# Kernel tuning notes

Hardware: AMD Instinct MI355X
Metric: run time of the kernel (lower is better)

The kernel has to match this reference:

```python
import jax, jax.numpy as jnp
import numpy as np

B, S, D, H = 2, 2048, 1024, 16
HD = D // H  # head_dim = 64


def setup_inputs() -> dict:
    key = jax.random.key(0)
    ks = jax.random.split(key, 6)
    std = 0.02
    return {
        "x": jax.random.normal(ks[0], (B, S, D), dtype=jnp.float32),
        "gamma": jnp.ones((D,), jnp.float32),
        "beta": jnp.zeros((D,), jnp.float32),
        "w_qkv": jax.random.normal(ks[1], (D, 3 * D), jnp.float32) * std,
        "b_qkv": jnp.zeros((3 * D,), jnp.float32),
        "w_out": jax.random.normal(ks[2], (D, D), jnp.float32) * std,
        "b_out": jnp.zeros((D,), jnp.float32),
        "w_gate": jax.random.normal(ks[3], (D, D), jnp.float32) * std,
        "b_gate": jnp.zeros((D,), jnp.float32),
    }


def reference(x, gamma, beta, w_qkv, b_qkv, w_out, b_out, w_gate, b_gate):
    residual = x
    # Pre-norm (LayerNorm over last dim, eps matches torch default 1e-5)
    mu = jnp.mean(x, axis=-1, keepdims=True)
    var = jnp.mean(jnp.square(x - mu), axis=-1, keepdims=True)
    xn = (x - mu) * jax.lax.rsqrt(var + 1e-5) * gamma + beta

    # Fused QKV projection: [B,S,3D] -> [B,S,3,H,HD]
    qkv = (xn @ w_qkv + b_qkv).reshape(B, S, 3, H, HD)
    q = qkv[:, :, 0].transpose(0, 2, 1, 3)  # [B,H,S,HD]
    k = qkv[:, :, 1].transpose(0, 2, 1, 3)
    v = qkv[:, :, 2].transpose(0, 2, 1, 3)

    scale = 1.0 / jnp.sqrt(jnp.float32(HD))
    scores = jnp.einsum("bhqd,bhkd->bhqk", q, k) * scale  # [B,H,S,S]
    attn = jax.nn.softmax(scores, axis=-1)  # dropout is identity in eval
    ctx = jnp.einsum("bhqk,bhkd->bhqd", attn, v)  # [B,H,S,HD]
    ctx = ctx.transpose(0, 2, 1, 3).reshape(B, S, D)

    out = ctx @ w_out + b_out
    gate = jax.nn.sigmoid(xn @ w_gate + b_gate)
    return out * gate + residual
```

## Files before the change

kernel.cpp:

```cpp
#include <hip/hip_runtime.h>

using u16 = unsigned short;
typedef __attribute__((ext_vector_type(8))) short bf16x8;
typedef __attribute__((ext_vector_type(4))) float f32x4;

constexpr int Bc = 2, Sc = 2048, Dc = 1024, Hc = 16;
constexpr int Mc = Bc * Sc;
constexpr int N3 = 3 * Dc;

__device__ __forceinline__ u16 f2bf(float f) {
  unsigned u = __float_as_uint(f);
  u += 0x7fffu + ((u >> 16) & 1u);
  return (u16)(u >> 16);
}

__device__ __forceinline__ void gload16(const void* g, void* l) {
  __builtin_amdgcn_global_load_lds(
      (const __attribute__((address_space(1))) void*)g,
      (__attribute__((address_space(3))) void*)l, 16, 0, 0);
}

__device__ __forceinline__ int swz(int row, int slot) {
  return row * 64 + ((slot ^ (row & 7)) << 3);
}

__global__ __launch_bounds__(256) void ln_kernel(
    const float* __restrict__ x, const float* __restrict__ gamma,
    const float* __restrict__ beta, u16* __restrict__ xn) {
  __shared__ float sred[8];
  const int row = blockIdx.x, tid = threadIdx.x;
  const float4 a = ((const float4*)(x + (size_t)row * Dc))[tid];
  float s = a.x + a.y + a.z + a.w;
  float ss = a.x * a.x + a.y * a.y + a.z * a.z + a.w * a.w;
#pragma unroll
  for (int off = 32; off; off >>= 1) {
    s += __shfl_xor(s, off, 64);
    ss += __shfl_xor(ss, off, 64);
  }
  const int wid = tid >> 6, lane = tid & 63;
  if (lane == 0) { sred[wid] = s; sred[4 + wid] = ss; }
  __syncthreads();
  s = sred[0] + sred[1] + sred[2] + sred[3];
  ss = sred[4] + sred[5] + sred[6] + sred[7];
  const float mean = s * (1.0f / Dc);
  const float rstd = rsqrtf(ss * (1.0f / Dc) - mean * mean + 1e-5f);
  const float4 g = ((const float4*)gamma)[tid];
  const float4 b = ((const float4*)beta)[tid];
  ushort4 o;
  o.x = f2bf((a.x - mean) * rstd * g.x + b.x);
  o.y = f2bf((a.y - mean) * rstd * g.y + b.y);
  o.z = f2bf((a.z - mean) * rstd * g.z + b.z);
  o.w = f2bf((a.w - mean) * rstd * g.w + b.w);
  *(ushort4*)(xn + (size_t)row * Dc + tid * 4) = o;
}

__global__ __launch_bounds__(256) void convertT(
    const float* __restrict__ W, u16* __restrict__ WT, int K, int N) {
  __shared__ float t[32][33];
  const int k0 = blockIdx.y * 32, n0 = blockIdx.x * 32;
  const int tid = threadIdx.x;
  const int r = tid >> 3, c4 = (tid & 7) << 2;
  const float4 v = *(const float4*)(W + (size_t)(k0 + r) * N + n0 + c4);
  t[r][c4 + 0] = v.x; t[r][c4 + 1] = v.y; t[r][c4 + 2] = v.z; t[r][c4 + 3] = v.w;
  __syncthreads();
  ushort4 o;
  o.x = f2bf(t[c4 + 0][r]); o.y = f2bf(t[c4 + 1][r]);
  o.z = f2bf(t[c4 + 2][r]); o.w = f2bf(t[c4 + 3][r]);
  *(ushort4*)(WT + (size_t)(n0 + r) * K + k0 + c4) = o;
}

__global__ __launch_bounds__(256) void gemm_qkv_kernel(
    const u16* __restrict__ A, const u16* __restrict__ BT,
    const float* __restrict__ bias, u16* __restrict__ Qb,
    u16* __restrict__ Kb, u16* __restrict__ VbT) {
  __shared__ __align__(16) u16 Al[128 * 64];
  __shared__ __align__(16) u16 Bl[128 * 64];
  const int tid = threadIdx.x, wv = tid >> 6, ln = tid & 63;
  const int bm = blockIdx.y * 128, bn = blockIdx.x * 128;
  const int wr = (wv >> 1) * 64, wc = (wv & 1) * 64;

  f32x4 acc[4][4];
#pragma unroll
  for (int i = 0; i < 4; i++)
#pragma unroll
    for (int j = 0; j < 4; j++) acc[i][j] = f32x4{0.f, 0.f, 0.f, 0.f};

  for (int k0 = 0; k0 < Dc; k0 += 64) {
    __syncthreads();
#pragma unroll
    for (int c = 0; c < 4; c++) {
      const int ci = wv + c * 4;
      const int i = ci * 64 + ln;
      const int row = i >> 3, slot = i & 7;
      const size_t go = (size_t)row * Dc + k0 + ((slot ^ (row & 7)) << 3);
      gload16(A + (size_t)bm * Dc + go, &Al[ci * 512]);
      gload16(BT + (size_t)bn * Dc + go, &Bl[ci * 512]);
    }
    __syncthreads();
#pragma unroll
    for (int ks = 0; ks < 2; ks++) {
      bf16x8 af[4], bfr[4];
#pragma unroll
      for (int m = 0; m < 4; m++)
        af[m] = *(const bf16x8*)&Al[swz(wr + m * 16 + (ln & 15), ks * 4 + (ln >> 4))];
#pragma unroll
      for (int n = 0; n < 4; n++)
        bfr[n] = *(const bf16x8*)&Bl[swz(wc + n * 16 + (ln & 15), ks * 4 + (ln >> 4))];
#pragma unroll
      for (int m = 0; m < 4; m++)
#pragma unroll
        for (int n = 0; n < 4; n++)
          acc[m][n] = __builtin_amdgcn_mfma_f32_16x16x32_bf16(af[m], bfr[n], acc[m][n], 0, 0, 0);
    }
  }

  const int fq = ln >> 4, fr = ln & 15;
#pragma unroll
  for (int mi = 0; mi < 4; mi++) {
    const int row = bm + wr + mi * 16 + fq * 4;
    const int b = row >> 11, sl = row & 2047;
#pragma unroll
    for (int ni = 0; ni < 4; ni++) {
      const int col = bn + wc + ni * 16 + fr;
      const int which = col >> 10, h = (col >> 6) & 15, hd = col & 63;
      const int bh = b * Hc + h;
      const float bs = bias[col];
      if (which == 0) {
#pragma unroll
        for (int r = 0; r < 4; r++)
          Qb[((size_t)bh * Sc + sl + r) * 64 + hd] = f2bf((acc[mi][ni][r] + bs) * 0.125f);
      } else if (which == 1) {
#pragma unroll
        for (int r = 0; r < 4; r++)
          Kb[((size_t)bh * Sc + sl + r) * 64 + hd] = f2bf(acc[mi][ni][r] + bs);
      } else {
        ushort4 st;
        st.x = f2bf(acc[mi][ni][0] + bs); st.y = f2bf(acc[mi][ni][1] + bs);
        st.z = f2bf(acc[mi][ni][2] + bs); st.w = f2bf(acc[mi][ni][3] + bs);
        *(ushort4*)&VbT[((size_t)bh * 64 + hd) * Sc + sl] = st;
      }
    }
  }
}

__global__ __launch_bounds__(256) void attn_kernel(
    const u16* __restrict__ Qb, const u16* __restrict__ Kb,
    const u16* __restrict__ VbT, u16* __restrict__ ctx) {
  __shared__ __align__(16) u16 Ks[64 * 64];
  __shared__ __align__(16) u16 Vs[64 * 64];
  __shared__ __align__(16) u16 Pl[4][16 * 64];
  const int tid = threadIdx.x, wv = tid >> 6, ln = tid & 63;
  const int qt = blockIdx.x, bh = blockIdx.y;
  const int b = bh >> 4, h = bh & 15;
  const int q0 = qt * 64 + wv * 16;

  bf16x8 qf[2];
  {
    const u16* Qrow = Qb + ((size_t)bh * Sc + q0 + (ln & 15)) * 64;
    qf[0] = *(const bf16x8*)(Qrow + ((ln >> 4) << 3));
    qf[1] = *(const bf16x8*)(Qrow + 32 + ((ln >> 4) << 3));
  }

  f32x4 O[4];
  float m_[4], l_[4];
#pragma unroll
  for (int f = 0; f < 4; f++) O[f] = f32x4{0.f, 0.f, 0.f, 0.f};
#pragma unroll
  for (int r = 0; r < 4; r++) { m_[r] = -1e30f; l_[r] = 0.f; }

  const u16* Kbase = Kb + (size_t)bh * Sc * 64;
  const u16* Vbase = VbT + (size_t)bh * 64 * Sc;
  u16* Pw = &Pl[wv][0];

  for (int kt = 0; kt < Sc / 64; kt++) {
    __syncthreads();
#pragma unroll
    for (int c = 0; c < 2; c++) {
      const int ci = wv + c * 4;
      const int i = ci * 64 + ln;
      const int row = i >> 3, slot = i & 7;
      const int so = (slot ^ (row & 7)) << 3;
      gload16(Kbase + ((size_t)kt * 64 + row) * 64 + so, &Ks[ci * 512]);
      gload16(Vbase + (size_t)row * Sc + kt * 64 + so, &Vs[ci * 512]);
    }
    __syncthreads();

    f32x4 sf[4];
#pragma unroll
    for (int f = 0; f < 4; f++) {
      f32x4 s = f32x4{0.f, 0.f, 0.f, 0.f};
#pragma unroll
      for (int ks = 0; ks < 2; ks++) {
        bf16x8 kf = *(const bf16x8*)&Ks[swz(f * 16 + (ln & 15), ks * 4 + (ln >> 4))];
        s = __builtin_amdgcn_mfma_f32_16x16x32_bf16(qf[ks], kf, s, 0, 0, 0);
      }
      sf[f] = s;
    }

    float al[4];
#pragma unroll
    for (int r = 0; r < 4; r++) {
      float v = fmaxf(fmaxf(sf[0][r], sf[1][r]), fmaxf(sf[2][r], sf[3][r]));
#pragma unroll
      for (int o = 1; o < 16; o <<= 1) v = fmaxf(v, __shfl_xor(v, o, 16));
      const float mn = fmaxf(m_[r], v);
      al[r] = __expf(m_[r] - mn);
      m_[r] = mn;
    }
    float rs[4] = {0.f, 0.f, 0.f, 0.f};
#pragma unroll
    for (int f = 0; f < 4; f++)
#pragma unroll
      for (int r = 0; r < 4; r++) {
        const float p = __expf(sf[f][r] - m_[r]);
        sf[f][r] = p;
        rs[r] += p;
      }
#pragma unroll
    for (int r = 0; r < 4; r++) {
#pragma unroll
      for (int o = 1; o < 16; o <<= 1) rs[r] += __shfl_xor(rs[r], o, 16);
      l_[r] = l_[r] * al[r] + rs[r];
    }
#pragma unroll
    for (int f = 0; f < 4; f++)
#pragma unroll
      for (int r = 0; r < 4; r++) O[f][r] *= al[r];

#pragma unroll
    for (int f = 0; f < 4; f++)
#pragma unroll
      for (int r = 0; r < 4; r++) {
        const int row = (ln >> 4) * 4 + r, key = f * 16 + (ln & 15);
        Pw[row * 64 + (key ^ ((row & 7) << 3))] = f2bf(sf[f][r]);
      }
    asm volatile("s_waitcnt lgkmcnt(0)" ::: "memory");

#pragma unroll
    for (int f = 0; f < 4; f++)
#pragma unroll
      for (int ks = 0; ks < 2; ks++) {
        bf16x8 pa = *(const bf16x8*)&Pw[swz(ln & 15, ks * 4 + (ln >> 4))];
        bf16x8 vb = *(const bf16x8*)&Vs[swz(f * 16 + (ln & 15), ks * 4 + (ln >> 4))];
        O[f] = __builtin_amdgcn_mfma_f32_16x16x32_bf16(pa, vb, O[f], 0, 0, 0);
      }
  }

#pragma unroll
  for (int r = 0; r < 4; r++) l_[r] = 1.0f / l_[r];
#pragma unroll
  for (int f = 0; f < 4; f++)
#pragma unroll
    for (int r = 0; r < 4; r++) {
      const int row = q0 + (ln >> 4) * 4 + r;
      ctx[((size_t)b * Sc + row) * Dc + h * 64 + f * 16 + (ln & 15)] =
          f2bf(O[f][r] * l_[r]);
    }
}

__global__ __launch_bounds__(256) void final_kernel(
    const u16* __restrict__ ctx, const u16* __restrict__ xn,
    const u16* __restrict__ woutT, const u16* __restrict__ wgateT,
    const float* __restrict__ b_out, const float* __restrict__ b_gate,
    const float* __restrict__ x, float* __restrict__ out) {
  __shared__ __align__(16) u16 A1[64 * 64], A2[64 * 64], B1[64 * 64], B2[64 * 64];
  const int tid = threadIdx.x, wv = tid >> 6, ln = tid & 63;
  const int bm = blockIdx.y * 64, bn = blockIdx.x * 64;
  const int wr = (wv >> 1) * 32, wc = (wv & 1) * 32;

  f32x4 ac1[2][2], ac2[2][2];
#pragma unroll
  for (int i = 0; i < 2; i++)
#pragma unroll
    for (int j = 0; j < 2; j++) {
      ac1[i][j] = f32x4{0.f, 0.f, 0.f, 0.f};
      ac2[i][j] = f32x4{0.f, 0.f, 0.f, 0.f};
    }

  for (int k0 = 0; k0 < Dc; k0 += 64) {
    __syncthreads();
#pragma unroll
    for (int c = 0; c < 2; c++) {
      const int ci = wv + c * 4;
      const int i = ci * 64 + ln;
      const int row = i >> 3, slot = i & 7;
      const size_t go = (size_t)row * Dc + k0 + ((slot ^ (row & 7)) << 3);
      gload16(ctx + (size_t)bm * Dc + go, &A1[ci * 512]);
      gload16(xn + (size_t)bm * Dc + go, &A2[ci * 512]);
      gload16(woutT + (size_t)bn * Dc + go, &B1[ci * 512]);
      gload16(wgateT + (size_t)bn * Dc + go, &B2[ci * 512]);
    }
    __syncthreads();
#pragma unroll
    for (int ks = 0; ks < 2; ks++) {
      bf16x8 fa1[2], fa2[2], fb1[2], fb2[2];
#pragma unroll
      for (int m = 0; m < 2; m++) {
        const int off = swz(wr + m * 16 + (ln & 15), ks * 4 + (ln >> 4));
        fa1[m] = *(const bf16x8*)&A1[off];
        fa2[m] = *(const bf16x8*)&A2[off];
      }
#pragma unroll
      for (int n = 0; n < 2; n++) {
        const int off = swz(wc + n * 16 + (ln & 15), ks * 4 + (ln >> 4));
        fb1[n] = *(const bf16x8*)&B1[off];
        fb2[n] = *(const bf16x8*)&B2[off];
      }
#pragma unroll
      for (int m = 0; m < 2; m++)
#pragma unroll
        for (int n = 0; n < 2; n++) {
          ac1[m][n] = __builtin_amdgcn_mfma_f32_16x16x32_bf16(fa1[m], fb1[n], ac1[m][n], 0, 0, 0);
          ac2[m][n] = __builtin_amdgcn_mfma_f32_16x16x32_bf16(fa2[m], fb2[n], ac2[m][n], 0, 0, 0);
        }
    }
  }

  const int fq = ln >> 4, fr = ln & 15;
#pragma unroll
  for (int m = 0; m < 2; m++)
#pragma unroll
    for (int n = 0; n < 2; n++) {
      const int col = bn + wc + n * 16 + fr;
      const float bo = b_out[col], bg = b_gate[col];
#pragma unroll
      for (int r = 0; r < 4; r++) {
        const int row = bm + wr + m * 16 + fq * 4 + r;
        const float o = ac1[m][n][r] + bo;
        const float gv = ac2[m][n][r] + bg;
        const float sig = 1.0f / (1.0f + __expf(-gv));
        out[(size_t)row * Dc + col] = o * sig + x[(size_t)row * Dc + col];
      }
    }
}

extern "C" void kernel_launch(void* const* d_in, const int* in_sizes, int n_in,
                              void* d_out, int out_size, void* d_ws, size_t ws_size,
                              hipStream_t stream) {
  const float* x = (const float*)d_in[0];
  const float* gamma = (const float*)d_in[1];
  const float* beta = (const float*)d_in[2];
  const float* w_qkv = (const float*)d_in[3];
  const float* b_qkv = (const float*)d_in[4];
  const float* w_out = (const float*)d_in[5];
  const float* b_out = (const float*)d_in[6];
  const float* w_gate = (const float*)d_in[7];
  const float* b_gate = (const float*)d_in[8];
  float* out = (float*)d_out;

  u16* xn = (u16*)d_ws;
  u16* wqkvT = xn + (size_t)Mc * Dc;
  u16* woutT = wqkvT + (size_t)N3 * Dc;
  u16* wgateT = woutT + (size_t)Dc * Dc;
  u16* Qb = wgateT + (size_t)Dc * Dc;
  u16* Kb = Qb + (size_t)Bc * Hc * Sc * 64;
  u16* VbT = Kb + (size_t)Bc * Hc * Sc * 64;
  u16* ctxb = VbT + (size_t)Bc * Hc * Sc * 64;

  ln_kernel<<<Mc, 256, 0, stream>>>(x, gamma, beta, xn);
  convertT<<<dim3(N3 / 32, Dc / 32), 256, 0, stream>>>(w_qkv, wqkvT, Dc, N3);
  convertT<<<dim3(Dc / 32, Dc / 32), 256, 0, stream>>>(w_out, woutT, Dc, Dc);
  convertT<<<dim3(Dc / 32, Dc / 32), 256, 0, stream>>>(w_gate, wgateT, Dc, Dc);
  gemm_qkv_kernel<<<dim3(N3 / 128, Mc / 128), 256, 0, stream>>>(
      xn, wqkvT, b_qkv, Qb, Kb, VbT);
  attn_kernel<<<dim3(Sc / 64, Bc * Hc), 256, 0, stream>>>(Qb, Kb, VbT, ctxb);
  final_kernel<<<dim3(Dc / 64, Mc / 64), 256, 0, stream>>>(
      ctxb, xn, woutT, wgateT, b_out, b_gate, x, out);
}
```

Measured before the change: 287.5 us.

## Double-buffer attention K/V, lazy softmax rescale, XCD swizzle, larger final tiles

The attention kernel now runs 2 waves per block, each handling 32 query rows, and double-buffers K/V tiles in LDS so the next tile loads while the current one is computed. Softmax uses exp2 with log2e folded into the Q scale, and only rescales the running max when it grows past a threshold. Row sums are reduced once at the end instead of every tile. The QKV and final GEMMs remap blocks across XCDs, and the final GEMM uses 128-row tiles. This trades more registers and LDS per block, and fewer threads per block, for better overlap of loads and compute and less softmax work.

```diff
diff --git a/kernel.cpp b/kernel.cpp
--- a/kernel.cpp
+++ b/kernel.cpp
@@ -22,6 +22,14 @@
 
 __device__ __forceinline__ int swz(int row, int slot) {
   return row * 64 + ((slot ^ (row & 7)) << 3);
+}
+
+__device__ __forceinline__ void xcd_swizzle(int& bx, int& by) {
+  const int nwg = gridDim.x * gridDim.y;
+  const int bid = by * gridDim.x + bx;
+  const int s = (bid & 7) * (nwg >> 3) + (bid >> 3);
+  bx = s % gridDim.x;
+  by = s / gridDim.x;
 }
 
 __global__ __launch_bounds__(256) void ln_kernel(
@@ -76,7 +84,9 @@
   __shared__ __align__(16) u16 Al[128 * 64];
   __shared__ __align__(16) u16 Bl[128 * 64];
   const int tid = threadIdx.x, wv = tid >> 6, ln = tid & 63;
-  const int bm = blockIdx.y * 128, bn = blockIdx.x * 128;
+  int bxi = blockIdx.x, byi = blockIdx.y;
+  xcd_swizzle(bxi, byi);
+  const int bm = byi * 128, bn = bxi * 128;
   const int wr = (wv >> 1) * 64, wc = (wv & 1) * 64;
 
   f32x4 acc[4][4];
@@ -128,7 +138,8 @@
       if (which == 0) {
 #pragma unroll
         for (int r = 0; r < 4; r++)
-          Qb[((size_t)bh * Sc + sl + r) * 64 + hd] = f2bf((acc[mi][ni][r] + bs) * 0.125f);
+          Qb[((size_t)bh * Sc + sl + r) * 64 + hd] =
+              f2bf((acc[mi][ni][r] + bs) * 0.18033688011112042f);
       } else if (which == 1) {
 #pragma unroll
         for (int r = 0; r < 4; r++)
@@ -143,119 +154,165 @@
   }
 }
 
-__global__ __launch_bounds__(256) void attn_kernel(
+__global__ __launch_bounds__(128) void attn_kernel(
     const u16* __restrict__ Qb, const u16* __restrict__ Kb,
     const u16* __restrict__ VbT, u16* __restrict__ ctx) {
-  __shared__ __align__(16) u16 Ks[64 * 64];
-  __shared__ __align__(16) u16 Vs[64 * 64];
-  __shared__ __align__(16) u16 Pl[4][16 * 64];
+  __shared__ __align__(16) u16 Ks[2][64 * 64];
+  __shared__ __align__(16) u16 Vs[2][64 * 64];
+  __shared__ __align__(16) u16 Pl[2][32 * 64];
   const int tid = threadIdx.x, wv = tid >> 6, ln = tid & 63;
   const int qt = blockIdx.x, bh = blockIdx.y;
   const int b = bh >> 4, h = bh & 15;
-  const int q0 = qt * 64 + wv * 16;
-
-  bf16x8 qf[2];
-  {
-    const u16* Qrow = Qb + ((size_t)bh * Sc + q0 + (ln & 15)) * 64;
-    qf[0] = *(const bf16x8*)(Qrow + ((ln >> 4) << 3));
-    qf[1] = *(const bf16x8*)(Qrow + 32 + ((ln >> 4) << 3));
-  }
-
-  f32x4 O[4];
-  float m_[4], l_[4];
-#pragma unroll
-  for (int f = 0; f < 4; f++) O[f] = f32x4{0.f, 0.f, 0.f, 0.f};
-#pragma unroll
-  for (int r = 0; r < 4; r++) { m_[r] = -1e30f; l_[r] = 0.f; }
+  const int q0 = qt * 64 + wv * 32;
+  constexpr float THR = 11.5f;
+
+  bf16x8 qf[2][2];
+#pragma unroll
+  for (int a = 0; a < 2; a++)
+#pragma unroll
+    for (int ks = 0; ks < 2; ks++)
+      qf[a][ks] = *(const bf16x8*)(Qb + ((size_t)bh * Sc + q0 + a * 16 + (ln & 15)) * 64 +
+                                   (ks * 4 + (ln >> 4)) * 8);
+
+  f32x4 O[2][4];
+  float m_[2][4], l_[2][4];
+#pragma unroll
+  for (int a = 0; a < 2; a++)
+#pragma unroll
+    for (int f = 0; f < 4; f++) O[a][f] = f32x4{0.f, 0.f, 0.f, 0.f};
+#pragma unroll
+  for (int a = 0; a < 2; a++)
+#pragma unroll
+    for (int r = 0; r < 4; r++) { m_[a][r] = -1e30f; l_[a][r] = 0.f; }
 
   const u16* Kbase = Kb + (size_t)bh * Sc * 64;
   const u16* Vbase = VbT + (size_t)bh * 64 * Sc;
   u16* Pw = &Pl[wv][0];
 
+  int rk[4], rv[4];
+#pragma unroll
+  for (int c = 0; c < 4; c++) {
+    const int ci = wv * 4 + c;
+    const int i = ci * 64 + ln;
+    const int row = i >> 3, slot = i & 7;
+    const int so = (slot ^ (row & 7)) << 3;
+    rk[c] = row * 64 + so;
+    rv[c] = row * Sc + so;
+  }
+
+  auto stage = [&](int buf, int kt) {
+#pragma unroll
+    for (int c = 0; c < 4; c++) {
+      const int ci = wv * 4 + c;
+      gload16(Kbase + (size_t)kt * 4096 + rk[c], &Ks[buf][ci * 512]);
+      gload16(Vbase + (size_t)kt * 64 + rv[c], &Vs[buf][ci * 512]);
+    }
+  };
+
+  stage(0, 0);
+  asm volatile("s_waitcnt vmcnt(0)" ::: "memory");
+  __syncthreads();
+
   for (int kt = 0; kt < Sc / 64; kt++) {
+    const int cur = kt & 1;
+    if (kt + 1 < Sc / 64) stage(cur ^ 1, kt + 1);
+
+    f32x4 sf[2][4];
+#pragma unroll
+    for (int a = 0; a < 2; a++)
+#pragma unroll
+      for (int f = 0; f < 4; f++) sf[a][f] = f32x4{0.f, 0.f, 0.f, 0.f};
+    __builtin_amdgcn_s_setprio(1);
+#pragma unroll
+    for (int f = 0; f < 4; f++)
+#pragma unroll
+      for (int ks = 0; ks < 2; ks++) {
+        const bf16x8 kf = *(const bf16x8*)&Ks[cur][swz(f * 16 + (ln & 15), ks * 4 + (ln >> 4))];
+#pragma unroll
+        for (int a = 0; a < 2; a++)
+          sf[a][f] = __builtin_amdgcn_mfma_f32_16x16x32_bf16(qf[a][ks], kf, sf[a][f], 0, 0, 0);
+      }
+    __builtin_amdgcn_s_setprio(0);
+
+    float pm[2][4];
+    bool need = false;
+#pragma unroll
+    for (int a = 0; a < 2; a++)
+#pragma unroll
+      for (int r = 0; r < 4; r++) {
+        pm[a][r] = fmaxf(fmaxf(sf[a][0][r], sf[a][1][r]), fmaxf(sf[a][2][r], sf[a][3][r]));
+        need |= pm[a][r] > m_[a][r] + THR;
+      }
+    if (__any(need)) {
+#pragma unroll
+      for (int a = 0; a < 2; a++)
+#pragma unroll
+        for (int r = 0; r < 4; r++) {
+          float v = pm[a][r];
+#pragma unroll
+          for (int o = 1; o < 16; o <<= 1) v = fmaxf(v, __shfl_xor(v, o, 16));
+          v = fmaxf(v, m_[a][r]);
+          const float al = exp2f(m_[a][r] - v);
+          m_[a][r] = v;
+          l_[a][r] *= al;
+#pragma unroll
+          for (int f = 0; f < 4; f++) O[a][f][r] *= al;
+        }
+    }
+#pragma unroll
+    for (int a = 0; a < 2; a++)
+#pragma unroll
+      for (int f = 0; f < 4; f++)
+#pragma unroll
+        for (int r = 0; r < 4; r++) {
+          const float p = exp2f(sf[a][f][r] - m_[a][r]);
+          l_[a][r] += p;
+          const int row = a * 16 + (ln >> 4) * 4 + r;
+          const int key = f * 16 + (ln & 15);
+          Pw[row * 64 + (key ^ ((row & 7) << 3))] = f2bf(p);
+        }
+    asm volatile("s_waitcnt lgkmcnt(0)" ::: "memory");
+
+    __builtin_amdgcn_s_setprio(1);
+#pragma unroll
+    for (int ks = 0; ks < 2; ks++) {
+      bf16x8 pa[2];
+#pragma unroll
+      for (int a = 0; a < 2; a++)
+        pa[a] = *(const bf16x8*)&Pw[swz(a * 16 + (ln & 15), ks * 4 + (ln >> 4))];
+#pragma unroll
+      for (int f = 0; f < 4; f++) {
+        const bf16x8 vb = *(const bf16x8*)&Vs[cur][swz(f * 16 + (ln & 15), ks * 4 + (ln >> 4))];
+#pragma unroll
+        for (int a = 0; a < 2; a++)
+          O[a][f] = __builtin_amdgcn_mfma_f32_16x16x32_bf16(pa[a], vb, O[a][f], 0, 0, 0);
+      }
+    }
+    __builtin_amdgcn_s_setprio(0);
+
+    asm volatile("s_waitcnt vmcnt(0)" ::: "memory");
     __syncthreads();
-#pragma unroll
-    for (int c = 0; c < 2; c++) {
-      const int ci = wv + c * 4;
-      const int i = ci * 64 + ln;
-      const int row = i >> 3, slot = i & 7;
-      const int so = (slot ^ (row & 7)) << 3;
-      gload16(Kbase + ((size_t)kt * 64 + row) * 64 + so, &Ks[ci * 512]);
-      gload16(Vbase + (size_t)row * Sc + kt * 64 + so, &Vs[ci * 512]);
-    }
-    __syncthreads();
-
-    f32x4 sf[4];
-#pragma unroll
-    for (int f = 0; f < 4; f++) {
-      f32x4 s = f32x4{0.f, 0.f, 0.f, 0.f};
-#pragma unroll
-      for (int ks = 0; ks < 2; ks++) {
-        bf16x8 kf = *(const bf16x8*)&Ks[swz(f * 16 + (ln & 15), ks * 4 + (ln >> 4))];
-        s = __builtin_amdgcn_mfma_f32_16x16x32_bf16(qf[ks], kf, s, 0, 0, 0);
-      }
-      sf[f] = s;
-    }
-
-    float al[4];
+  }
+
+#pragma unroll
+  for (int a = 0; a < 2; a++)
 #pragma unroll
     for (int r = 0; r < 4; r++) {
-      float v = fmaxf(fmaxf(sf[0][r], sf[1][r]), fmaxf(sf[2][r], sf[3][r]));
-#pragma unroll
-      for (int o = 1; o < 16; o <<= 1) v = fmaxf(v, __shfl_xor(v, o, 16));
-      const float mn = fmaxf(m_[r], v);
-      al[r] = __expf(m_[r] - mn);
-      m_[r] = mn;
-    }
-    float rs[4] = {0.f, 0.f, 0.f, 0.f};
+      float v = l_[a][r];
+#pragma unroll
+      for (int o = 1; o < 16; o <<= 1) v += __shfl_xor(v, o, 16);
+      l_[a][r] = 1.0f / v;
+    }
+#pragma unroll
+  for (int a = 0; a < 2; a++)
 #pragma unroll
     for (int f = 0; f < 4; f++)
 #pragma unroll
       for (int r = 0; r < 4; r++) {
-        const float p = __expf(sf[f][r] - m_[r]);
-        sf[f][r] = p;
-        rs[r] += p;
-      }
-#pragma unroll
-    for (int r = 0; r < 4; r++) {
-#pragma unroll
-      for (int o = 1; o < 16; o <<= 1) rs[r] += __shfl_xor(rs[r], o, 16);
-      l_[r] = l_[r] * al[r] + rs[r];
-    }
-#pragma unroll
-    for (int f = 0; f < 4; f++)
-#pragma unroll
-      for (int r = 0; r < 4; r++) O[f][r] *= al[r];
-
-#pragma unroll
-    for (int f = 0; f < 4; f++)
-#pragma unroll
-      for (int r = 0; r < 4; r++) {
-        const int row = (ln >> 4) * 4 + r, key = f * 16 + (ln & 15);
-        Pw[row * 64 + (key ^ ((row & 7) << 3))] = f2bf(sf[f][r]);
-      }
-    asm volatile("s_waitcnt lgkmcnt(0)" ::: "memory");
-
-#pragma unroll
-    for (int f = 0; f < 4; f++)
-#pragma unroll
-      for (int ks = 0; ks < 2; ks++) {
-        bf16x8 pa = *(const bf16x8*)&Pw[swz(ln & 15, ks * 4 + (ln >> 4))];
-        bf16x8 vb = *(const bf16x8*)&Vs[swz(f * 16 + (ln & 15), ks * 4 + (ln >> 4))];
-        O[f] = __builtin_amdgcn_mfma_f32_16x16x32_bf16(pa, vb, O[f], 0, 0, 0);
-      }
-  }
-
-#pragma unroll
-  for (int r = 0; r < 4; r++) l_[r] = 1.0f / l_[r];
-#pragma unroll
-  for (int f = 0; f < 4; f++)
-#pragma unroll
-    for (int r = 0; r < 4; r++) {
-      const int row = q0 + (ln >> 4) * 4 + r;
-      ctx[((size_t)b * Sc + row) * Dc + h * 64 + f * 16 + (ln & 15)] =
-          f2bf(O[f][r] * l_[r]);
-    }
+        const int row = q0 + a * 16 + (ln >> 4) * 4 + r;
+        ctx[((size_t)b * Sc + row) * Dc + h * 64 + f * 16 + (ln & 15)] =
+            f2bf(O[a][f][r] * l_[a][r]);
+      }
 }
 
 __global__ __launch_bounds__(256) void final_kernel(
@@ -263,14 +320,17 @@
     const u16* __restrict__ woutT, const u16* __restrict__ wgateT,
     const float* __restrict__ b_out, const float* __restrict__ b_gate,
     const float* __restrict__ x, float* __restrict__ out) {
-  __shared__ __align__(16) u16 A1[64 * 64], A2[64 * 64], B1[64 * 64], B2[64 * 64];
+  __shared__ __align__(16) u16 A1[128 * 64], A2[128 * 64];
+  __shared__ __align__(16) u16 B1[64 * 64], B2[64 * 64];
   const int tid = threadIdx.x, wv = tid >> 6, ln = tid & 63;
-  const int bm = blockIdx.y * 64, bn = blockIdx.x * 64;
-  const int wr = (wv >> 1) * 32, wc = (wv & 1) * 32;
-
-  f32x4 ac1[2][2], ac2[2][2];
-#pragma unroll
-  for (int i = 0; i < 2; i++)
+  int bxi = blockIdx.x, byi = blockIdx.y;
+  xcd_swizzle(bxi, byi);
+  const int bm = byi * 128, bn = bxi * 64;
+  const int wr = (wv >> 1) * 64, wc = (wv & 1) * 32;
+
+  f32x4 ac1[4][2], ac2[4][2];
+#pragma unroll
+  for (int i = 0; i < 4; i++)
 #pragma unroll
     for (int j = 0; j < 2; j++) {
       ac1[i][j] = f32x4{0.f, 0.f, 0.f, 0.f};
@@ -280,22 +340,29 @@
   for (int k0 = 0; k0 < Dc; k0 += 64) {
     __syncthreads();
 #pragma unroll
-    for (int c = 0; c < 2; c++) {
+    for (int c = 0; c < 4; c++) {
       const int ci = wv + c * 4;
       const int i = ci * 64 + ln;
       const int row = i >> 3, slot = i & 7;
       const size_t go = (size_t)row * Dc + k0 + ((slot ^ (row & 7)) << 3);
       gload16(ctx + (size_t)bm * Dc + go, &A1[ci * 512]);
       gload16(xn + (size_t)bm * Dc + go, &A2[ci * 512]);
+    }
+#pragma unroll
+    for (int c = 0; c < 2; c++) {
+      const int ci = wv + c * 4;
+      const int i = ci * 64 + ln;
+      const int row = i >> 3, slot = i & 7;
+      const size_t go = (size_t)row * Dc + k0 + ((slot ^ (row & 7)) << 3);
       gload16(woutT + (size_t)bn * Dc + go, &B1[ci * 512]);
       gload16(wgateT + (size_t)bn * Dc + go, &B2[ci * 512]);
     }
     __syncthreads();
 #pragma unroll
     for (int ks = 0; ks < 2; ks++) {
-      bf16x8 fa1[2], fa2[2], fb1[2], fb2[2];
-#pragma unroll
-      for (int m = 0; m < 2; m++) {
+      bf16x8 fa1[4], fa2[4], fb1[2], fb2[2];
+#pragma unroll
+      for (int m = 0; m < 4; m++) {
         const int off = swz(wr + m * 16 + (ln & 15), ks * 4 + (ln >> 4));
         fa1[m] = *(const bf16x8*)&A1[off];
         fa2[m] = *(const bf16x8*)&A2[off];
@@ -307,7 +374,7 @@
         fb2[n] = *(const bf16x8*)&B2[off];
       }
 #pragma unroll
-      for (int m = 0; m < 2; m++)
+      for (int m = 0; m < 4; m++)
 #pragma unroll
         for (int n = 0; n < 2; n++) {
           ac1[m][n] = __builtin_amdgcn_mfma_f32_16x16x32_bf16(fa1[m], fb1[n], ac1[m][n], 0, 0, 0);
@@ -318,7 +385,7 @@
 
   const int fq = ln >> 4, fr = ln & 15;
 #pragma unroll
-  for (int m = 0; m < 2; m++)
+  for (int m = 0; m < 4; m++)
 #pragma unroll
     for (int n = 0; n < 2; n++) {
       const int col = bn + wc + n * 16 + fr;
@@ -363,7 +430,7 @@
   convertT<<<dim3(Dc / 32, Dc / 32), 256, 0, stream>>>(w_gate, wgateT, Dc, Dc);
   gemm_qkv_kernel<<<dim3(N3 / 128, Mc / 128), 256, 0, stream>>>(
       xn, wqkvT, b_qkv, Qb, Kb, VbT);
-  attn_kernel<<<dim3(Sc / 64, Bc * Hc), 256, 0, stream>>>(Qb, Kb, VbT, ctxb);
-  final_kernel<<<dim3(Dc / 64, Mc / 64), 256, 0, stream>>>(
+  attn_kernel<<<dim3(Sc / 64, Bc * Hc), 128, 0, stream>>>(Qb, Kb, VbT, ctxb);
+  final_kernel<<<dim3(Dc / 64, Mc / 128), 256, 0, stream>>>(
       ctxb, xn, woutT, wgateT, b_out, b_gate, x, out);
 }
```

New measurement: 270.7 us. -5.8%, faster.
